# Optimization experiments

Hardware: AMD Instinct MI355X
Metric: run time of the kernel (lower is better)

The kernel has to match this reference:

```python
import jax, jax.numpy as jnp
import numpy as np

B, C, H, W = 4, 512, 64, 64
CQ = C // 8  # 64 channels for each of query/key projections


def conv1x1(t, w, b):
    # t: [B, Cin, H, W], w: [Cout, Cin], b: [Cout]
    return jnp.einsum('bchw,oc->bohw', t, w) + b[None, :, None, None]


def setup_inputs() -> dict:
    key = jax.random.key(0)
    ks = jax.random.split(key, 12)
    s = 0.05
    return {
        'x':   jax.random.normal(ks[0], (B, C, H, W), jnp.float32),
        'dep': jax.random.normal(ks[1], (B, C, H, W), jnp.float32),
        'wq':  jax.random.normal(ks[2], (CQ, C), jnp.float32) * s,
        'bq':  jnp.zeros((CQ,), jnp.float32),
        'wqd': jax.random.normal(ks[3], (CQ, C), jnp.float32) * s,
        'bqd': jnp.zeros((CQ,), jnp.float32),
        'wk':  jax.random.normal(ks[4], (CQ, C), jnp.float32) * s,
        'bk':  jnp.zeros((CQ,), jnp.float32),
        'wkd': jax.random.normal(ks[5], (CQ, C), jnp.float32) * s,
        'bkd': jnp.zeros((CQ,), jnp.float32),
        'wv':  jax.random.normal(ks[6], (C, C), jnp.float32) * s,
        'bv':  jnp.zeros((C,), jnp.float32),
        'gamma': jnp.full((1,), 0.5, jnp.float32),
    }


def reference(x, dep, wq, bq, wqd, bqd, wk, bk, wkd, bkd, wv, bv, gamma):
    b, c, h, w = x.shape
    n = h * w
    # concatenated RGB+depth query/key projections: [B, 2*CQ, N]
    q = jnp.concatenate([conv1x1(x, wq, bq), conv1x1(dep, wqd, bqd)], axis=1).reshape(b, -1, n)
    k = jnp.concatenate([conv1x1(x, wk, bk), conv1x1(dep, wkd, bkd)], axis=1).reshape(b, -1, n)
    # energy[b, i, j] = sum_d q[b, d, i] * k[b, d, j]  -> [B, N, N]
    energy = jnp.einsum('bdi,bdj->bij', q, k)
    attn = jax.nn.softmax(energy, axis=-1)
    v = conv1x1(x, wv, bv).reshape(b, c, n)  # [B, C, N]
    # out[b, c, i] = sum_j v[b, c, j] * attn[b, i, j]
    out = jnp.einsum('bcj,bij->bci', v, attn).reshape(b, c, h, w)
    return gamma.reshape(()) * out + x
```

## Files before the change

kernel.cpp:

```cpp
#include <hip/hip_runtime.h>


typedef __attribute__((ext_vector_type(8))) short bf16x8;
typedef __attribute__((ext_vector_type(4))) float f32x4;

__device__ __forceinline__ float bf2f(unsigned short u) {
  return __builtin_bit_cast(float, (unsigned int)u << 16);
}
__device__ __forceinline__ unsigned short f2bf(float f) {
  unsigned int u = __builtin_bit_cast(unsigned int, f);
  u = u + 0x7fffu + ((u >> 16) & 1u);
  return (unsigned short)(u >> 16);
}
__device__ __forceinline__ float bflo(unsigned int u) {
  return __builtin_bit_cast(float, u << 16);
}

__device__ __forceinline__ void gld16(const char* g, char* l) {
  __builtin_amdgcn_global_load_lds(
      (const __attribute__((address_space(1))) unsigned int*)g,
      (__attribute__((address_space(3))) unsigned int*)l, 16, 0, 0);
}

__device__ __forceinline__ int detect_fp32_mode(const void* xv) {
  const unsigned int* p = (const unsigned int*)xv;
  const int lane = threadIdx.x & 63;
  const unsigned int w0 = p[lane];
  const unsigned int w1 = p[64 + lane];
  int cnt = 0;
  const unsigned short us[4] = {
      (unsigned short)(w0 & 0xffffu), (unsigned short)(w0 >> 16),
      (unsigned short)(w1 & 0xffffu), (unsigned short)(w1 >> 16)};
#pragma unroll
  for (int h = 0; h < 4; ++h) {
    const float a = fabsf(bf2f(us[h]));
    cnt += (a > 9.0e-13f && a < 32.0f) ? 1 : 0;
  }
#pragma unroll
  for (int mm = 32; mm >= 1; mm >>= 1) cnt += __shfl_xor(cnt, mm, 64);
  return cnt < 220;
}

__global__ __launch_bounds__(256) void prep_kernel(
    const void* wq, const void* bq, const void* wqd, const void* bqd,
    const void* wk, const void* bk, const void* wkd, const void* bkd,
    const void* wv, const void* bv, const void* gam, const void* x,
    unsigned short* __restrict__ Whi, unsigned short* __restrict__ Wlo,
    float* __restrict__ Bcat, float* __restrict__ gamF)
{
  const int fp32mode = detect_fp32_mode(x);
  const int row = blockIdx.x;
  const void* src; const void* bsrc; int srow;
  if (row < 64)       { src = wq;  bsrc = bq;  srow = row; }
  else if (row < 128) { src = wqd; bsrc = bqd; srow = row - 64; }
  else if (row < 192) { src = wk;  bsrc = bk;  srow = row - 128; }
  else if (row < 256) { src = wkd; bsrc = bkd; srow = row - 192; }
  else                { src = wv;  bsrc = bv;  srow = row - 256; }
  for (int c = threadIdx.x; c < 512; c += 256) {
    const float v = fp32mode ? ((const float*)src)[(size_t)srow * 512 + c]
                             : bf2f(((const unsigned short*)src)[(size_t)srow * 512 + c]);
    const unsigned short h = f2bf(v);
    Whi[(size_t)row * 512 + c] = h;
    Wlo[(size_t)row * 512 + c] = f2bf(v - bf2f(h));
  }
  if (threadIdx.x == 0) {
    Bcat[row] = fp32mode ? ((const float*)bsrc)[srow]
                         : bf2f(((const unsigned short*)bsrc)[srow]);
    if (row == 0)
      gamF[0] = fp32mode ? ((const float*)gam)[0]
                         : bf2f(((const unsigned short*)gam)[0]);
  }
}

__device__ __forceinline__ void do_tile2(
    const unsigned short* __restrict__ Whi, const unsigned short* __restrict__ Wlo,
    const float* bsh,
    const unsigned short* Xhi, const unsigned short* Xlo, int fp32mode,
    int wrow0, int kind, int d0,
    int b, int n0, int l15, int quad,
    unsigned short* __restrict__ Qhi, unsigned short* __restrict__ Qlo,
    unsigned short* __restrict__ Kst, unsigned short* __restrict__ Vst)
{
  f32x4 a0, a1;
#pragma unroll
  for (int r = 0; r < 4; ++r) a0[r] = a1[r] = bsh[wrow0 + quad * 4 + r];
  const unsigned short* whi = Whi + (size_t)(wrow0 + l15) * 512;
  const unsigned short* wlo = Wlo + (size_t)(wrow0 + l15) * 512;
  const unsigned short* x0h = Xhi + l15 * 520;
  const unsigned short* x1h = Xhi + (16 + l15) * 520;
  const unsigned short* x0l = Xlo + l15 * 520;
  const unsigned short* x1l = Xlo + (16 + l15) * 520;
#pragma unroll
  for (int ks = 0; ks < 16; ++ks) {
    const int o = ks * 32 + quad * 8;
    const bf16x8 ah = *(const bf16x8*)(whi + o);
    const bf16x8 b0 = *(const bf16x8*)(x0h + o);
    const bf16x8 b1 = *(const bf16x8*)(x1h + o);
    a0 = __builtin_amdgcn_mfma_f32_16x16x32_bf16(ah, b0, a0, 0, 0, 0);
    a1 = __builtin_amdgcn_mfma_f32_16x16x32_bf16(ah, b1, a1, 0, 0, 0);
    if (fp32mode) {
      const bf16x8 al_ = *(const bf16x8*)(wlo + o);
      const bf16x8 c0 = *(const bf16x8*)(x0l + o);
      const bf16x8 c1 = *(const bf16x8*)(x1l + o);
      a0 = __builtin_amdgcn_mfma_f32_16x16x32_bf16(ah, c0, a0, 0, 0, 0);
      a0 = __builtin_amdgcn_mfma_f32_16x16x32_bf16(al_, b0, a0, 0, 0, 0);
      a1 = __builtin_amdgcn_mfma_f32_16x16x32_bf16(ah, c1, a1, 0, 0, 0);
      a1 = __builtin_amdgcn_mfma_f32_16x16x32_bf16(al_, b1, a1, 0, 0, 0);
    }
  }
#pragma unroll
  for (int ns = 0; ns < 2; ++ns) {
    const f32x4 acc = ns ? a1 : a0;
    const int n = n0 + ns * 16 + l15;
    if (kind <= 1) {
      ushort4 h, l;
#pragma unroll
      for (int r = 0; r < 4; ++r) {
        const float f = acc[r];
        const unsigned short hh = f2bf(f);
        ((unsigned short*)&h)[r] = hh;
        ((unsigned short*)&l)[r] = f2bf(f - bf2f(hh));
      }
      if (kind == 0) {
        const size_t base = (((size_t)b << 12) + n) * 128 + d0 + quad * 4;
        *(ushort4*)(Qhi + base) = h;
        *(ushort4*)(Qlo + base) = l;
      } else {
        const int t = n >> 5, j = n & 31, d = d0 + quad * 4;
        char* tb = (char*)Kst + (((size_t)b * 128 + t) << 14);
        const unsigned off =
            ((unsigned)((j * 128 + d) * 2)) ^ ((unsigned)(j & 7) << 4);
        *(ushort4*)(tb + off) = h;
        *(ushort4*)(tb + 8192 + off) = l;
      }
    } else {
      const int t = n >> 5, j = n & 31;
      char* tb = (char*)Vst + (((size_t)b * 128 + t) << 15);
#pragma unroll
      for (int r = 0; r < 4; ++r) {
        const int c = d0 + quad * 4 + r;
        const unsigned off =
            ((unsigned)((c * 32 + j) * 2)) ^ ((unsigned)(c & 7) << 4);
        *(unsigned short*)(tb + off) = f2bf(acc[r]);
      }
    }
  }
}

__global__ __launch_bounds__(512, 4) void proj_kernel(
    const void* __restrict__ x, const void* __restrict__ dep,
    const unsigned short* __restrict__ Whi, const unsigned short* __restrict__ Wlo,
    const float* __restrict__ Bcat,
    unsigned short* __restrict__ Qhi, unsigned short* __restrict__ Qlo,
    unsigned short* __restrict__ Kst, unsigned short* __restrict__ Vst)
{
  __shared__ unsigned short Xhi[32 * 520];
  __shared__ unsigned short Xlo[32 * 520];
  __shared__ float bsh[768];
  const int fp32mode = detect_fp32_mode(x);
  const int tid  = threadIdx.x;
  const int lane = tid & 63;
  const int w    = tid >> 6;
  const int l15  = lane & 15;
  const int quad = lane >> 4;
  const int b  = blockIdx.y;
  const int n0 = blockIdx.x * 32;

  const int cbase = tid >> 4;
  const int nn    = (tid & 15) * 2;

  for (int i = tid; i < 768; i += 512) bsh[i] = Bcat[i];

  for (int r = 0; r < 16; ++r) {
    const int c = cbase + r * 32;
    const size_t off = (((size_t)b * 512 + c) << 12) + n0 + nn;
    float v0, v1;
    if (fp32mode) {
      const float2 f2 = *(const float2*)((const float*)x + off);
      v0 = f2.x; v1 = f2.y;
    } else {
      const unsigned int v2 = *(const unsigned int*)((const unsigned short*)x + off);
      v0 = bflo(v2 & 0xffffu); v1 = bflo(v2 >> 16);
    }
    const unsigned short h0 = f2bf(v0), h1 = f2bf(v1);
    Xhi[nn * 520 + c]       = h0;
    Xhi[(nn + 1) * 520 + c] = h1;
    Xlo[nn * 520 + c]       = f2bf(v0 - bf2f(h0));
    Xlo[(nn + 1) * 520 + c] = f2bf(v1 - bf2f(h1));
  }
  __syncthreads();

  for (int rt = w; rt < 40; rt += 8) {
    if (rt < 4)
      do_tile2(Whi, Wlo, bsh, Xhi, Xlo, fp32mode, rt * 16,             0, rt * 16,
               b, n0, l15, quad, Qhi, Qlo, Kst, Vst);
    else if (rt < 8)
      do_tile2(Whi, Wlo, bsh, Xhi, Xlo, fp32mode, 128 + (rt - 4) * 16, 1, (rt - 4) * 16,
               b, n0, l15, quad, Qhi, Qlo, Kst, Vst);
    else
      do_tile2(Whi, Wlo, bsh, Xhi, Xlo, fp32mode, 256 + (rt - 8) * 16, 2, (rt - 8) * 16,
               b, n0, l15, quad, Qhi, Qlo, Kst, Vst);
  }
  __syncthreads();

  for (int r = 0; r < 16; ++r) {
    const int c = cbase + r * 32;
    const size_t off = (((size_t)b * 512 + c) << 12) + n0 + nn;
    float v0, v1;
    if (fp32mode) {
      const float2 f2 = *(const float2*)((const float*)dep + off);
      v0 = f2.x; v1 = f2.y;
    } else {
      const unsigned int v2 = *(const unsigned int*)((const unsigned short*)dep + off);
      v0 = bflo(v2 & 0xffffu); v1 = bflo(v2 >> 16);
    }
    const unsigned short h0 = f2bf(v0), h1 = f2bf(v1);
    Xhi[nn * 520 + c]       = h0;
    Xhi[(nn + 1) * 520 + c] = h1;
    Xlo[nn * 520 + c]       = f2bf(v0 - bf2f(h0));
    Xlo[(nn + 1) * 520 + c] = f2bf(v1 - bf2f(h1));
  }
  __syncthreads();

  {
    const int rt = w;
    if (rt < 4)
      do_tile2(Whi, Wlo, bsh, Xhi, Xlo, fp32mode, 64 + rt * 16,        0, 64 + rt * 16,
               b, n0, l15, quad, Qhi, Qlo, Kst, Vst);
    else
      do_tile2(Whi, Wlo, bsh, Xhi, Xlo, fp32mode, 192 + (rt - 4) * 16, 1, 64 + (rt - 4) * 16,
               b, n0, l15, quad, Qhi, Qlo, Kst, Vst);
  }
}

__global__ __launch_bounds__(512, 2) void attn_kernel(
    const unsigned short* __restrict__ Qhi, const unsigned short* __restrict__ Qlo,
    const unsigned short* __restrict__ Kst, const unsigned short* __restrict__ Vst,
    const void* __restrict__ x, const float* __restrict__ gamF,
    void* __restrict__ outp)
{
  __shared__ char KL[2][16384];
  __shared__ char VL[2][32768];
  __shared__ unsigned short P[64][48];
  __shared__ float lstat[4][2][16];

  const int fp32mode = detect_fp32_mode(x);
  const int tid  = threadIdx.x;
  const int lane = tid & 63;
  const int w    = tid >> 6;
  const int l15  = lane & 15;
  const int quad = lane >> 4;
  const int itE  = w >> 1;
  const int jt   = w & 1;
  const int ih   = w >> 2;
  const int cq   = w & 3;
  const int id   = blockIdx.x;
  const int b    = (id >> 1) & 3;
  const int n0   = (((id >> 3) << 1) | (id & 1)) * 64;

  bf16x8 qh[4], ql[4];
  {
    const size_t qb = (((size_t)b << 12) + n0 + itE * 16 + l15) * 128 + quad * 8;
#pragma unroll
    for (int ds = 0; ds < 4; ++ds) {
      qh[ds] = *(const bf16x8*)(Qhi + qb + ds * 32);
      ql[ds] = *(const bf16x8*)(Qlo + qb + ds * 32);
    }
  }

  const char* Kb = (const char*)Kst + (((size_t)b * 128) << 14);
  const char* Vb = (const char*)Vst + (((size_t)b * 128) << 15);

  {
#pragma unroll
    for (int ch = 0; ch < 2; ++ch) {
      const int c = w + ch * 8;
      gld16(Kb + c * 1024 + lane * 16, &KL[0][c * 1024]);
    }
#pragma unroll
    for (int ch = 0; ch < 4; ++ch) {
      const int c = w + ch * 8;
      gld16(Vb + c * 1024 + lane * 16, &VL[0][c * 1024]);
    }
  }

  f32x4 acc[8][2];
#pragma unroll
  for (int ct = 0; ct < 8; ++ct)
#pragma unroll
    for (int itv = 0; itv < 2; ++itv) acc[ct][itv] = (f32x4){0.f, 0.f, 0.f, 0.f};
  float lpart = 0.f;

  for (int t = 0; t < 128; ++t) {
    const int cur = t & 1, nxt = cur ^ 1;
    if (t < 127) {
      const char* src = Kb + ((size_t)(t + 1) << 14);
#pragma unroll
      for (int ch = 0; ch < 2; ++ch) {
        const int c = w + ch * 8;
        gld16(src + c * 1024 + lane * 16, &KL[nxt][c * 1024]);
      }
      __builtin_amdgcn_sched_barrier(0);
      asm volatile("s_waitcnt vmcnt(6)" ::: "memory");
    } else {
      asm volatile("s_waitcnt vmcnt(4)" ::: "memory");
    }
    __builtin_amdgcn_sched_barrier(0);
    __builtin_amdgcn_s_barrier();
    __builtin_amdgcn_sched_barrier(0);
    if (t < 127) {
      const char* src = Vb + ((size_t)(t + 1) << 15);
#pragma unroll
      for (int ch = 0; ch < 4; ++ch) {
        const int c = w + ch * 8;
        gld16(src + c * 1024 + lane * 16, &VL[nxt][c * 1024]);
      }
    }
    {
      const int row = jt * 16 + l15;
      const unsigned rsw = (unsigned)(row & 7) << 4;
      const char* kb = &KL[cur][0];
      bf16x8 kh[4], kl[4];
#pragma unroll
      for (int ds = 0; ds < 4; ++ds) {
        const unsigned off = ((unsigned)(row * 256 + quad * 16 + ds * 64)) ^ rsw;
        kh[ds] = *(const bf16x8*)(kb + off);
        kl[ds] = *(const bf16x8*)(kb + 8192 + off);
      }
      f32x4 ea = (f32x4){0.f, 0.f, 0.f, 0.f};
      f32x4 eb = (f32x4){0.f, 0.f, 0.f, 0.f};
      f32x4 ec = (f32x4){0.f, 0.f, 0.f, 0.f};
      __builtin_amdgcn_s_setprio(1);
#pragma unroll
      for (int ds = 0; ds < 4; ++ds) {
        ea = __builtin_amdgcn_mfma_f32_16x16x32_bf16(kh[ds], qh[ds], ea, 0, 0, 0);
        eb = __builtin_amdgcn_mfma_f32_16x16x32_bf16(kh[ds], ql[ds], eb, 0, 0, 0);
        ec = __builtin_amdgcn_mfma_f32_16x16x32_bf16(kl[ds], qh[ds], ec, 0, 0, 0);
      }
      __builtin_amdgcn_s_setprio(0);
      const f32x4 e = (ea + eb) + ec;
      const float p0 = __expf(e[0] - 32.0f);
      const float p1 = __expf(e[1] - 32.0f);
      const float p2 = __expf(e[2] - 32.0f);
      const float p3 = __expf(e[3] - 32.0f);
      const unsigned short u0 = f2bf(p0), u1 = f2bf(p1);
      const unsigned short u2 = f2bf(p2), u3 = f2bf(p3);
      lpart += (bf2f(u0) + bf2f(u1)) + (bf2f(u2) + bf2f(u3));
      uint2 pk;
      pk.x = (unsigned int)u0 | ((unsigned int)u1 << 16);
      pk.y = (unsigned int)u2 | ((unsigned int)u3 << 16);
      *(uint2*)(&P[itE * 16 + l15][jt * 16 + quad * 4]) = pk;
    }
    __builtin_amdgcn_sched_barrier(0);
    if (t < 127)
      asm volatile("s_waitcnt vmcnt(6) lgkmcnt(0)" ::: "memory");
    else
      asm volatile("s_waitcnt vmcnt(0) lgkmcnt(0)" ::: "memory");
    __builtin_amdgcn_sched_barrier(0);
    __builtin_amdgcn_s_barrier();
    __builtin_amdgcn_sched_barrier(0);
    {
      bf16x8 pf[2];
#pragma unroll
      for (int itv = 0; itv < 2; ++itv)
        pf[itv] = *(const bf16x8*)(&P[ih * 32 + itv * 16 + l15][quad * 8]);
      const char* vb = &VL[cur][0];
      __builtin_amdgcn_s_setprio(1);
#pragma unroll
      for (int ct = 0; ct < 8; ++ct) {
        const int c = cq * 128 + ct * 16 + l15;
        const unsigned off =
            ((unsigned)(c * 64 + quad * 16)) ^ ((unsigned)(c & 7) << 4);
        const bf16x8 va = *(const bf16x8*)(vb + off);
        acc[ct][0] = __builtin_amdgcn_mfma_f32_16x16x32_bf16(va, pf[0], acc[ct][0], 0, 0, 0);
        acc[ct][1] = __builtin_amdgcn_mfma_f32_16x16x32_bf16(va, pf[1], acc[ct][1], 0, 0, 0);
      }
      __builtin_amdgcn_s_setprio(0);
    }
  }

  {
    float lp = lpart;
    lp += __shfl_xor(lp, 16, 64);
    lp += __shfl_xor(lp, 32, 64);
    if (quad == 0) lstat[itE][jt][l15] = lp;
  }
  __syncthreads();

  const float gv = gamF[0];
  float sc[2];
#pragma unroll
  for (int itv = 0; itv < 2; ++itv) {
    const int itg = ih * 2 + itv;
    const float l = lstat[itg][0][l15] + lstat[itg][1][l15];
    sc[itv] = gv / l;
  }
#pragma unroll
  for (int ct = 0; ct < 8; ++ct)
#pragma unroll
    for (int r = 0; r < 4; ++r) {
      const int c_g = cq * 128 + ct * 16 + quad * 4 + r;
      const size_t brow = ((size_t)b * 512 + c_g) << 12;
#pragma unroll
      for (int itv = 0; itv < 2; ++itv) {
        const size_t addr = brow + n0 + ih * 32 + itv * 16 + l15;
        const float o = sc[itv] * acc[ct][itv][r];
        if (fp32mode) {
          ((float*)outp)[addr] = o + ((const float*)x)[addr];
        } else {
          ((unsigned short*)outp)[addr] =
              f2bf(o + bf2f(((const unsigned short*)x)[addr]));
        }
      }
    }
}

extern "C" void kernel_launch(void* const* d_in, const int* in_sizes, int n_in,
                              void* d_out, int out_size, void* d_ws, size_t ws_size,
                              hipStream_t stream) {
  const void* x    = d_in[0];
  const void* dep  = d_in[1];
  const void* wq   = d_in[2];
  const void* bq   = d_in[3];
  const void* wqd  = d_in[4];
  const void* bqd  = d_in[5];
  const void* wk   = d_in[6];
  const void* bk   = d_in[7];
  const void* wkd  = d_in[8];
  const void* bkd  = d_in[9];
  const void* wv   = d_in[10];
  const void* bv   = d_in[11];
  const void* gam  = d_in[12];

  unsigned short* Whi = (unsigned short*)d_ws;
  unsigned short* Wlo = Whi + (size_t)768 * 512;
  float* Bcat = (float*)(Wlo + (size_t)768 * 512);
  float* gamF = Bcat + 768;
  unsigned short* Qhi = (unsigned short*)((char*)d_ws + ((size_t)2 << 20));
  unsigned short* Qlo = (unsigned short*)((char*)d_ws + ((size_t)6 << 20));
  unsigned short* Kst = (unsigned short*)((char*)d_ws + ((size_t)10 << 20));
  unsigned short* Vst = (unsigned short*)((char*)d_ws + ((size_t)18 << 20));

  prep_kernel<<<768, 256, 0, stream>>>(wq, bq, wqd, bqd, wk, bk, wkd, bkd,
                                       wv, bv, gam, x, Whi, Wlo, Bcat, gamF);
  proj_kernel<<<dim3(128, 4), 512, 0, stream>>>(x, dep, Whi, Wlo, Bcat,
                                                Qhi, Qlo, Kst, Vst);
  attn_kernel<<<256, 512, 0, stream>>>(Qhi, Qlo, Kst, Vst, x, gamF, d_out);
}
```

Measured before the change: 420.4 us.

## Warp-specialize attention into QK/softmax producer waves and PV consumer waves

Splits the attention block into 4 producer waves that compute QK energies, exp and the row-sum partials, and 8 consumer waves that run the P·V MFMAs. They are linked through a double-buffered P tile in LDS, with the consumers one step behind. The aim is to overlap the energy/exp work with the PV accumulation instead of alternating both phases across all waves. Block size grows to 768 and launch bounds become (768,3). That bound caps registers per thread tightly while each consumer wave holds a 4x4 accumulator set, so spilling is a risk, and LDS usage still allows only one block per CU.

```diff
diff --git a/kernel.cpp b/kernel.cpp
--- a/kernel.cpp
+++ b/kernel.cpp
@@ -233,7 +233,7 @@
   }
 }
 
-__global__ __launch_bounds__(512, 2) void attn_kernel(
+__global__ __launch_bounds__(768, 3) void attn_kernel(
     const unsigned short* __restrict__ Qhi, const unsigned short* __restrict__ Qlo,
     const unsigned short* __restrict__ Kst, const unsigned short* __restrict__ Vst,
     const void* __restrict__ x, const float* __restrict__ gamF,
@@ -241,8 +241,8 @@
 {
   __shared__ char KL[2][16384];
   __shared__ char VL[2][32768];
-  __shared__ unsigned short P[64][48];
-  __shared__ float lstat[4][2][16];
+  __shared__ unsigned short P[2][64][40];
+  __shared__ float lstat[2][4][16];
 
   const int fp32mode = detect_fp32_mode(x);
   const int tid  = threadIdx.x;
@@ -250,160 +250,175 @@
   const int w    = tid >> 6;
   const int l15  = lane & 15;
   const int quad = lane >> 4;
-  const int itE  = w >> 1;
-  const int jt   = w & 1;
-  const int ih   = w >> 2;
-  const int cq   = w & 3;
   const int id   = blockIdx.x;
   const int b    = (id >> 1) & 3;
   const int n0   = (((id >> 3) << 1) | (id & 1)) * 64;
 
-  bf16x8 qh[4], ql[4];
-  {
-    const size_t qb = (((size_t)b << 12) + n0 + itE * 16 + l15) * 128 + quad * 8;
-#pragma unroll
-    for (int ds = 0; ds < 4; ++ds) {
-      qh[ds] = *(const bf16x8*)(Qhi + qb + ds * 32);
-      ql[ds] = *(const bf16x8*)(Qlo + qb + ds * 32);
-    }
-  }
+  asm volatile("" :: "v"(fp32mode) : "memory");
 
   const char* Kb = (const char*)Kst + (((size_t)b * 128) << 14);
   const char* Vb = (const char*)Vst + (((size_t)b * 128) << 15);
 
-  {
-#pragma unroll
-    for (int ch = 0; ch < 2; ++ch) {
-      const int c = w + ch * 8;
+  if (w < 4) {
+    const int ihE = w >> 1;
+    const int jt  = w & 1;
+    bf16x8 qh[2][4], ql[2][4];
+#pragma unroll
+    for (int itq = 0; itq < 2; ++itq) {
+      const size_t qb =
+          (((size_t)b << 12) + n0 + ihE * 32 + itq * 16 + l15) * 128 + quad * 8;
+#pragma unroll
+      for (int ds = 0; ds < 4; ++ds) {
+        qh[itq][ds] = *(const bf16x8*)(Qhi + qb + ds * 32);
+        ql[itq][ds] = *(const bf16x8*)(Qlo + qb + ds * 32);
+      }
+    }
+#pragma unroll
+    for (int ch = 0; ch < 4; ++ch) {
+      const int c = w + ch * 4;
       gld16(Kb + c * 1024 + lane * 16, &KL[0][c * 1024]);
     }
-#pragma unroll
-    for (int ch = 0; ch < 4; ++ch) {
-      const int c = w + ch * 8;
-      gld16(Vb + c * 1024 + lane * 16, &VL[0][c * 1024]);
-    }
-  }
-
-  f32x4 acc[8][2];
-#pragma unroll
-  for (int ct = 0; ct < 8; ++ct)
-#pragma unroll
-    for (int itv = 0; itv < 2; ++itv) acc[ct][itv] = (f32x4){0.f, 0.f, 0.f, 0.f};
-  float lpart = 0.f;
-
-  for (int t = 0; t < 128; ++t) {
-    const int cur = t & 1, nxt = cur ^ 1;
-    if (t < 127) {
-      const char* src = Kb + ((size_t)(t + 1) << 14);
-#pragma unroll
-      for (int ch = 0; ch < 2; ++ch) {
-        const int c = w + ch * 8;
-        gld16(src + c * 1024 + lane * 16, &KL[nxt][c * 1024]);
-      }
+    float lpart[2] = {0.f, 0.f};
+
+    for (int t = 0; t <= 128; ++t) {
+      asm volatile("s_waitcnt vmcnt(0) lgkmcnt(0)" ::: "memory");
       __builtin_amdgcn_sched_barrier(0);
-      asm volatile("s_waitcnt vmcnt(6)" ::: "memory");
-    } else {
+      __builtin_amdgcn_s_barrier();
+      __builtin_amdgcn_sched_barrier(0);
+      if (t < 128) {
+        const int cur = t & 1;
+        if (t < 127) {
+          const char* src = Kb + ((size_t)(t + 1) << 14);
+#pragma unroll
+          for (int ch = 0; ch < 4; ++ch) {
+            const int c = w + ch * 4;
+            gld16(src + c * 1024 + lane * 16, &KL[cur ^ 1][c * 1024]);
+          }
+        }
+        __builtin_amdgcn_sched_barrier(0);
+        const int row = jt * 16 + l15;
+        const unsigned rsw = (unsigned)(row & 7) << 4;
+        const char* kb = &KL[cur][0];
+        bf16x8 kh[4], kl[4];
+#pragma unroll
+        for (int ds = 0; ds < 4; ++ds) {
+          const unsigned off = ((unsigned)(row * 256 + quad * 16 + ds * 64)) ^ rsw;
+          kh[ds] = *(const bf16x8*)(kb + off);
+          kl[ds] = *(const bf16x8*)(kb + 8192 + off);
+        }
+        f32x4 ea[2], eb[2], ec[2];
+#pragma unroll
+        for (int itq = 0; itq < 2; ++itq) {
+          ea[itq] = (f32x4){0.f, 0.f, 0.f, 0.f};
+          eb[itq] = (f32x4){0.f, 0.f, 0.f, 0.f};
+          ec[itq] = (f32x4){0.f, 0.f, 0.f, 0.f};
+        }
+        __builtin_amdgcn_s_setprio(1);
+#pragma unroll
+        for (int ds = 0; ds < 4; ++ds)
+#pragma unroll
+          for (int itq = 0; itq < 2; ++itq) {
+            ea[itq] = __builtin_amdgcn_mfma_f32_16x16x32_bf16(kh[ds], qh[itq][ds], ea[itq], 0, 0, 0);
+            eb[itq] = __builtin_amdgcn_mfma_f32_16x16x32_bf16(kh[ds], ql[itq][ds], eb[itq], 0, 0, 0);
+            ec[itq] = __builtin_amdgcn_mfma_f32_16x16x32_bf16(kl[ds], qh[itq][ds], ec[itq], 0, 0, 0);
+          }
+        __builtin_amdgcn_s_setprio(0);
+#pragma unroll
+        for (int itq = 0; itq < 2; ++itq) {
+          const f32x4 e = (ea[itq] + eb[itq]) + ec[itq];
+          const float p0 = __expf(e[0] - 32.0f);
+          const float p1 = __expf(e[1] - 32.0f);
+          const float p2 = __expf(e[2] - 32.0f);
+          const float p3 = __expf(e[3] - 32.0f);
+          const unsigned short u0 = f2bf(p0), u1 = f2bf(p1);
+          const unsigned short u2 = f2bf(p2), u3 = f2bf(p3);
+          lpart[itq] += (bf2f(u0) + bf2f(u1)) + (bf2f(u2) + bf2f(u3));
+          unsigned int* dst = (unsigned int*)
+              (&P[cur][ihE * 32 + itq * 16 + l15][jt * 16 + quad * 4]);
+          dst[0] = (unsigned int)u0 | ((unsigned int)u1 << 16);
+          dst[1] = (unsigned int)u2 | ((unsigned int)u3 << 16);
+        }
+      }
+    }
+#pragma unroll
+    for (int itq = 0; itq < 2; ++itq) {
+      float lp = lpart[itq];
+      lp += __shfl_xor(lp, 16, 64);
+      lp += __shfl_xor(lp, 32, 64);
+      if (quad == 0) lstat[jt][ihE * 2 + itq][l15] = lp;
+    }
+    __syncthreads();
+    return;
+  }
+
+  const int wv = w - 4;
+#pragma unroll
+  for (int k = 0; k < 4; ++k) {
+    const int c = wv * 4 + k;
+    gld16(Vb + c * 1024 + lane * 16, &VL[0][c * 1024]);
+  }
+  f32x4 acc[4][4];
+#pragma unroll
+  for (int ct = 0; ct < 4; ++ct)
+#pragma unroll
+    for (int itv = 0; itv < 4; ++itv) acc[ct][itv] = (f32x4){0.f, 0.f, 0.f, 0.f};
+
+  for (int t = 0; t <= 128; ++t) {
+    if (t <= 127)
       asm volatile("s_waitcnt vmcnt(4)" ::: "memory");
-    }
+    else
+      asm volatile("s_waitcnt vmcnt(0)" ::: "memory");
     __builtin_amdgcn_sched_barrier(0);
     __builtin_amdgcn_s_barrier();
     __builtin_amdgcn_sched_barrier(0);
-    if (t < 127) {
-      const char* src = Vb + ((size_t)(t + 1) << 15);
-#pragma unroll
-      for (int ch = 0; ch < 4; ++ch) {
-        const int c = w + ch * 8;
-        gld16(src + c * 1024 + lane * 16, &VL[nxt][c * 1024]);
-      }
-    }
-    {
-      const int row = jt * 16 + l15;
-      const unsigned rsw = (unsigned)(row & 7) << 4;
-      const char* kb = &KL[cur][0];
-      bf16x8 kh[4], kl[4];
-#pragma unroll
-      for (int ds = 0; ds < 4; ++ds) {
-        const unsigned off = ((unsigned)(row * 256 + quad * 16 + ds * 64)) ^ rsw;
-        kh[ds] = *(const bf16x8*)(kb + off);
-        kl[ds] = *(const bf16x8*)(kb + 8192 + off);
-      }
-      f32x4 ea = (f32x4){0.f, 0.f, 0.f, 0.f};
-      f32x4 eb = (f32x4){0.f, 0.f, 0.f, 0.f};
-      f32x4 ec = (f32x4){0.f, 0.f, 0.f, 0.f};
+    if (t >= 1) {
+      const int pb = (t - 1) & 1;
+      bf16x8 pf[4];
+#pragma unroll
+      for (int itv = 0; itv < 4; ++itv)
+        pf[itv] = *(const bf16x8*)(&P[pb][itv * 16 + l15][quad * 8]);
+      const char* vb = &VL[pb][0];
       __builtin_amdgcn_s_setprio(1);
 #pragma unroll
-      for (int ds = 0; ds < 4; ++ds) {
-        ea = __builtin_amdgcn_mfma_f32_16x16x32_bf16(kh[ds], qh[ds], ea, 0, 0, 0);
-        eb = __builtin_amdgcn_mfma_f32_16x16x32_bf16(kh[ds], ql[ds], eb, 0, 0, 0);
-        ec = __builtin_amdgcn_mfma_f32_16x16x32_bf16(kl[ds], qh[ds], ec, 0, 0, 0);
-      }
-      __builtin_amdgcn_s_setprio(0);
-      const f32x4 e = (ea + eb) + ec;
-      const float p0 = __expf(e[0] - 32.0f);
-      const float p1 = __expf(e[1] - 32.0f);
-      const float p2 = __expf(e[2] - 32.0f);
-      const float p3 = __expf(e[3] - 32.0f);
-      const unsigned short u0 = f2bf(p0), u1 = f2bf(p1);
-      const unsigned short u2 = f2bf(p2), u3 = f2bf(p3);
-      lpart += (bf2f(u0) + bf2f(u1)) + (bf2f(u2) + bf2f(u3));
-      uint2 pk;
-      pk.x = (unsigned int)u0 | ((unsigned int)u1 << 16);
-      pk.y = (unsigned int)u2 | ((unsigned int)u3 << 16);
-      *(uint2*)(&P[itE * 16 + l15][jt * 16 + quad * 4]) = pk;
-    }
-    __builtin_amdgcn_sched_barrier(0);
-    if (t < 127)
-      asm volatile("s_waitcnt vmcnt(6) lgkmcnt(0)" ::: "memory");
-    else
-      asm volatile("s_waitcnt vmcnt(0) lgkmcnt(0)" ::: "memory");
-    __builtin_amdgcn_sched_barrier(0);
-    __builtin_amdgcn_s_barrier();
-    __builtin_amdgcn_sched_barrier(0);
-    {
-      bf16x8 pf[2];
-#pragma unroll
-      for (int itv = 0; itv < 2; ++itv)
-        pf[itv] = *(const bf16x8*)(&P[ih * 32 + itv * 16 + l15][quad * 8]);
-      const char* vb = &VL[cur][0];
-      __builtin_amdgcn_s_setprio(1);
-#pragma unroll
-      for (int ct = 0; ct < 8; ++ct) {
-        const int c = cq * 128 + ct * 16 + l15;
+      for (int ct = 0; ct < 4; ++ct) {
+        const int c = wv * 64 + ct * 16 + l15;
         const unsigned off =
             ((unsigned)(c * 64 + quad * 16)) ^ ((unsigned)(c & 7) << 4);
         const bf16x8 va = *(const bf16x8*)(vb + off);
-        acc[ct][0] = __builtin_amdgcn_mfma_f32_16x16x32_bf16(va, pf[0], acc[ct][0], 0, 0, 0);
-        acc[ct][1] = __builtin_amdgcn_mfma_f32_16x16x32_bf16(va, pf[1], acc[ct][1], 0, 0, 0);
+#pragma unroll
+        for (int itv = 0; itv < 4; ++itv)
+          acc[ct][itv] = __builtin_amdgcn_mfma_f32_16x16x32_bf16(va, pf[itv], acc[ct][itv], 0, 0, 0);
       }
       __builtin_amdgcn_s_setprio(0);
-    }
-  }
-
-  {
-    float lp = lpart;
-    lp += __shfl_xor(lp, 16, 64);
-    lp += __shfl_xor(lp, 32, 64);
-    if (quad == 0) lstat[itE][jt][l15] = lp;
+      __builtin_amdgcn_sched_barrier(0);
+    }
+    if (t < 127) {
+      const char* src = Vb + ((size_t)(t + 1) << 15);
+#pragma unroll
+      for (int k = 0; k < 4; ++k) {
+        const int c = wv * 4 + k;
+        gld16(src + c * 1024 + lane * 16, &VL[(t + 1) & 1][c * 1024]);
+      }
+    }
   }
   __syncthreads();
 
   const float gv = gamF[0];
-  float sc[2];
-#pragma unroll
-  for (int itv = 0; itv < 2; ++itv) {
-    const int itg = ih * 2 + itv;
-    const float l = lstat[itg][0][l15] + lstat[itg][1][l15];
+  float sc[4];
+#pragma unroll
+  for (int itv = 0; itv < 4; ++itv) {
+    const float l = lstat[0][itv][l15] + lstat[1][itv][l15];
     sc[itv] = gv / l;
   }
 #pragma unroll
-  for (int ct = 0; ct < 8; ++ct)
+  for (int ct = 0; ct < 4; ++ct)
 #pragma unroll
     for (int r = 0; r < 4; ++r) {
-      const int c_g = cq * 128 + ct * 16 + quad * 4 + r;
+      const int c_g = wv * 64 + ct * 16 + quad * 4 + r;
       const size_t brow = ((size_t)b * 512 + c_g) << 12;
 #pragma unroll
-      for (int itv = 0; itv < 2; ++itv) {
-        const size_t addr = brow + n0 + ih * 32 + itv * 16 + l15;
+      for (int itv = 0; itv < 4; ++itv) {
+        const size_t addr = brow + n0 + itv * 16 + l15;
         const float o = sc[itv] * acc[ct][itv][r];
         if (fp32mode) {
           ((float*)outp)[addr] = o + ((const float*)x)[addr];
@@ -445,5 +460,5 @@
                                        wv, bv, gam, x, Whi, Wlo, Bcat, gamF);
   proj_kernel<<<dim3(128, 4), 512, 0, stream>>>(x, dep, Whi, Wlo, Bcat,
                                                 Qhi, Qlo, Kst, Vst);
-  attn_kernel<<<256, 512, 0, stream>>>(Qhi, Qlo, Kst, Vst, x, gamF, d_out);
-}
+  attn_kernel<<<256, 768, 0, stream>>>(Qhi, Qlo, Kst, Vst, x, gamF, d_out);
+}
```

New measurement: 362.4 us. 1.16x faster.
